# Kernel optimization log

Hardware: AMD Instinct MI355X
Metric: run time of the kernel (lower is better)

Reference implementation:

```python
import jax, jax.numpy as jnp
from jax import lax
import numpy as np


def gru_last(seq, Wih, Whh, bih, bhh):
    """Run a torch-style GRU over seq [N, T, C] and return only h_T [N, H].

    Gate order matches torch.nn.GRU: (r, z, n);
    n = tanh(W_in x + b_in + r * (W_hn h + b_hn)).
    """
    N = seq.shape[0]
    H = Whh.shape[1]

    def step(h, x_t):
        gi = x_t @ Wih.T + bih          # [N, 3H]
        gh = h @ Whh.T + bhh            # [N, 3H]
        i_r, i_z, i_n = jnp.split(gi, 3, axis=-1)
        h_r, h_z, h_n = jnp.split(gh, 3, axis=-1)
        r = jax.nn.sigmoid(i_r + h_r)
        z = jax.nn.sigmoid(i_z + h_z)
        n = jnp.tanh(i_n + r * h_n)
        h_new = (1.0 - z) * n + z * h
        return h_new, None

    h0 = jnp.zeros((N, H), dtype=seq.dtype)
    hT, _ = lax.scan(step, h0, jnp.swapaxes(seq, 0, 1))  # scan over T
    return hT


def setup_inputs() -> dict:
    key = jax.random.key(0)
    ks = jax.random.split(key, 12)
    B, C, T, Fq, H = 8, 64, 256, 256, 128
    s = 0.05
    return {
        "x": jax.random.normal(ks[0], (B, C, T, Fq), dtype=jnp.float32),
        "Wih_t": jax.random.normal(ks[1], (3 * H, C), dtype=jnp.float32) * s,
        "Whh_t": jax.random.normal(ks[2], (3 * H, H), dtype=jnp.float32) * s,
        "bih_t": jax.random.normal(ks[3], (3 * H,), dtype=jnp.float32) * s,
        "bhh_t": jax.random.normal(ks[4], (3 * H,), dtype=jnp.float32) * s,
        "Wih_f": jax.random.normal(ks[5], (3 * H, C), dtype=jnp.float32) * s,
        "Whh_f": jax.random.normal(ks[6], (3 * H, H), dtype=jnp.float32) * s,
        "bih_f": jax.random.normal(ks[7], (3 * H,), dtype=jnp.float32) * s,
        "bhh_f": jax.random.normal(ks[8], (3 * H,), dtype=jnp.float32) * s,
        "Wp": jax.random.normal(ks[9], (C, H), dtype=jnp.float32) * s,
        "bp": jax.random.normal(ks[10], (C,), dtype=jnp.float32) * s,
    }


def reference(x, Wih_t, Whh_t, bih_t, bhh_t, Wih_f, Whh_f, bih_f, bhh_f, Wp, bp):
    B, C, T, Fq = x.shape
    H = Whh_t.shape[1]

    # time GRU: sequences of length T, one per (batch, freq)
    t_in = jnp.transpose(x, (0, 3, 2, 1)).reshape(B * Fq, T, C)
    h_t = gru_last(t_in, Wih_t, Whh_t, bih_t, bhh_t)          # [B*F, H]
    t_vec = jnp.transpose(h_t.reshape(B, Fq, H), (0, 2, 1))    # [B, H, F]

    # freq GRU: sequences of length F, one per (batch, time)
    f_in = jnp.transpose(x, (0, 2, 3, 1)).reshape(B * T, Fq, C)
    h_f = gru_last(f_in, Wih_f, Whh_f, bih_f, bhh_f)          # [B*T, H]
    f_vec = jnp.transpose(h_f.reshape(B, T, H), (0, 2, 1))    # [B, H, T]

    # t_feat [B,H,F,1] expanded along dim2 to T (requires F == T),
    # f_feat [B,H,T,1] expanded along dim3 to F; fused is constant along F.
    s = t_vec + f_vec                                          # [B, H, T]  (F == T)
    out_t = jnp.einsum("ch,bht->bct", Wp, s) + bp[None, :, None]  # 1x1 conv
    return jnp.broadcast_to(out_t[:, :, :, None], (B, C, T, Fq))
```

## Files before the change

kernel.cpp:

```cpp
#include <hip/hip_runtime.h>

#define B_ 8
#define C_ 64
#define T_ 256
#define F_ 256
#define H_ 128
#define TF_ (T_*F_)

typedef _Float16 half_t;
typedef _Float16 half8 __attribute__((ext_vector_type(8)));
typedef float float4v __attribute__((ext_vector_type(4)));

#if __has_builtin(__builtin_amdgcn_exp2f)
#define EXP2F(x) __builtin_amdgcn_exp2f(x)
#else
static __device__ inline float EXP2F(float x) { float r; asm("v_exp_f32 %0, %1" : "=v"(r) : "v"(x)); return r; }
#endif
#if __has_builtin(__builtin_amdgcn_rcpf)
#define RCPF(x) __builtin_amdgcn_rcpf(x)
#else
static __device__ inline float RCPF(float x) { float r; asm("v_rcp_f32 %0, %1" : "=v"(r) : "v"(x)); return r; }
#endif

#define LDS_BARRIER() asm volatile("s_waitcnt lgkmcnt(0)\n\ts_barrier" ::: "memory")

#define NEG_L2E  (-1.4426950408889634f)
#define NEG_2L2E (-2.8853900817779268f)

__global__ __launch_bounds__(256) void k_transpose(const float* __restrict__ x,
                                                   half_t* __restrict__ xt) {
    __shared__ float lds[64 * 68];
    int blk = blockIdx.x;
    int b   = blk >> 10;
    int tf0 = (blk & 1023) << 6;
    int tid = threadIdx.x;
    int s = tid & 15;
    int q = tid >> 4;
    const float* xp = x + (size_t)(b * C_) * TF_ + tf0 + s * 4;
#pragma unroll
    for (int i = 0; i < 4; ++i) {
        int c = q + i * 16;
        float4v v = *(const float4v*)(xp + (size_t)c * TF_);
#pragma unroll
        for (int j = 0; j < 4; ++j) lds[(s * 4 + j) * 68 + c] = v[j];
    }
    __syncthreads();
    int row = tid >> 2;
    int c0  = (tid & 3) << 4;
    half8 o0, o1;
#pragma unroll
    for (int kq = 0; kq < 4; ++kq) {
        float4v v = *(const float4v*)&lds[row * 68 + c0 + kq * 4];
#pragma unroll
        for (int j = 0; j < 4; ++j) {
            if (kq < 2) o0[kq * 4 + j] = (half_t)v[j];
            else        o1[(kq - 2) * 4 + j] = (half_t)v[j];
        }
    }
    half_t* op = xt + ((size_t)b * TF_ + tf0 + row) * C_ + c0;
    *(half8*)op       = o0;
    *(half8*)(op + 8) = o1;
}

__device__ inline half8 load_w8s(const float* __restrict__ p, float s) {
    half8 r;
#pragma unroll
    for (int k = 0; k < 8; ++k) r[k] = (half_t)(p[k] * s);
    return r;
}

#define MFMA(a, b, c) __builtin_amdgcn_mfma_f32_16x16x32_f16((a), (b), (c), 0, 0, 0)

__global__ __launch_bounds__(512, 2) void k_gru(
    const half_t* __restrict__ xt,
    const float* __restrict__ Wih_t, const float* __restrict__ Whh_t,
    const float* __restrict__ bih_t, const float* __restrict__ bhh_t,
    const float* __restrict__ Wih_f, const float* __restrict__ Whh_f,
    const float* __restrict__ bih_f, const float* __restrict__ bhh_f,
    float* __restrict__ h_t_out, float* __restrict__ h_f_out) {
    __shared__ half_t hbuf0[16 * 136];
    __shared__ half_t hbuf1[16 * 136];

    int tid  = threadIdx.x;
    int w    = tid >> 6;
    int lane = tid & 63;
    int nidx = lane & 15;
    int quad = lane >> 4;

    int bi  = blockIdx.x;
    bool isf = bi >= 128;
    int lbi = bi & 127;
    int b   = lbi >> 4;
    int g16 = (lbi & 15) << 4;

    const float* Wih = isf ? Wih_f : Wih_t;
    const float* Whh = isf ? Whh_f : Whh_t;
    const float* bih = isf ? bih_f : bih_t;
    const float* bhh = isf ? bhh_f : bhh_t;
    float* hout      = isf ? h_f_out : h_t_out;

    size_t Sm = isf ? (size_t)(F_ * C_) : (size_t)C_;
    size_t Ss = isf ? (size_t)C_ : (size_t)(F_ * C_);
    size_t abase = (size_t)b * TF_ * C_ + (size_t)g16 * Sm;

    int gr = w * 16 + nidx;
    int gz = gr + 128;
    int gn = gr + 256;
    int ko = quad * 8;

    half8 wir0 = load_w8s(Wih + gr * 64 + ko,      NEG_L2E);
    half8 wir1 = load_w8s(Wih + gr * 64 + 32 + ko, NEG_L2E);
    half8 wiz0 = load_w8s(Wih + gz * 64 + ko,      NEG_L2E);
    half8 wiz1 = load_w8s(Wih + gz * 64 + 32 + ko, NEG_L2E);
    half8 win0 = load_w8s(Wih + gn * 64 + ko,      NEG_2L2E);
    half8 win1 = load_w8s(Wih + gn * 64 + 32 + ko, NEG_2L2E);
    half8 whr[4], whz[4], whn[4];
#pragma unroll
    for (int kt = 0; kt < 4; ++kt) {
        whr[kt] = load_w8s(Whh + gr * 128 + kt * 32 + ko, NEG_L2E);
        whz[kt] = load_w8s(Whh + gz * 128 + kt * 32 + ko, NEG_L2E);
        whn[kt] = load_w8s(Whh + gn * 128 + kt * 32 + ko, NEG_2L2E);
    }
    float br  = NEG_L2E  * (bih[gr] + bhh[gr]);
    float bz  = NEG_L2E  * (bih[gz] + bhh[gz]);
    float bin = NEG_2L2E * bih[gn];
    float bhn = NEG_2L2E * bhh[gn];

    for (int idx = tid; idx < 16 * 136; idx += 512) hbuf0[idx] = (half_t)0.f;
    float h_old[4] = {0.f, 0.f, 0.f, 0.f};

    const half_t* ap = xt + abase + (size_t)nidx * Sm + ko;
    half8 xA0 = *(const half8*)ap;
    half8 xA1 = *(const half8*)(ap + 32);
    ap += Ss;
    half8 xB0 = *(const half8*)ap;
    half8 xB1 = *(const half8*)(ap + 32);
    ap += Ss;

    float4v xr = {br, br, br, br};
    float4v xz = {bz, bz, bz, bz};
    float4v xn = {bin, bin, bin, bin};
    xr = MFMA(xA0, wir0, xr); xr = MFMA(xA1, wir1, xr);
    xz = MFMA(xA0, wiz0, xz); xz = MFMA(xA1, wiz1, xz);
    xn = MFMA(xA0, win0, xn); xn = MFMA(xA1, win1, xn);
    LDS_BARRIER();

#define GRU_STEP(RBUF, WBUF, XC0, XC1, XP0, XP1)                                \
    {                                                                           \
        const half_t* hrow = (RBUF) + nidx * 136 + ko;                          \
        half8 ha0 = *(const half8*)(hrow);                                      \
        half8 ha1 = *(const half8*)(hrow + 32);                                 \
        half8 ha2 = *(const half8*)(hrow + 64);                                 \
        half8 ha3 = *(const half8*)(hrow + 96);                                 \
        XP0 = *(const half8*)ap;                                                \
        XP1 = *(const half8*)(ap + 32);                                         \
        ap += Ss;                                                               \
        float4v hr  = {0.f, 0.f, 0.f, 0.f};                                     \
        float4v hz  = {0.f, 0.f, 0.f, 0.f};                                     \
        float4v hna = {bhn, bhn, bhn, bhn};                                     \
        float4v hnb = {0.f, 0.f, 0.f, 0.f};                                     \
        xr  = MFMA(ha0, whr[0], xr);  xr  = MFMA(ha1, whr[1], xr);              \
        hr  = MFMA(ha2, whr[2], hr);  hr  = MFMA(ha3, whr[3], hr);              \
        xz  = MFMA(ha0, whz[0], xz);  xz  = MFMA(ha1, whz[1], xz);              \
        hz  = MFMA(ha2, whz[2], hz);  hz  = MFMA(ha3, whz[3], hz);              \
        hna = MFMA(ha0, whn[0], hna); hna = MFMA(ha1, whn[1], hna);             \
        hnb = MFMA(ha2, whn[2], hnb); hnb = MFMA(ha3, whn[3], hnb);             \
        _Pragma("unroll")                                                       \
        for (int rg = 0; rg < 4; ++rg) {                                        \
            float r  = RCPF(1.f + EXP2F(xr[rg] + hr[rg]));                      \
            float z  = RCPF(1.f + EXP2F(xz[rg] + hz[rg]));                      \
            float np = xn[rg] + r * (hna[rg] + hnb[rg]);                        \
            float n  = 2.f * RCPF(1.f + EXP2F(np)) - 1.f;                       \
            float h  = n + z * (h_old[rg] - n);                                 \
            h_old[rg] = h;                                                      \
            (WBUF)[(quad * 4 + rg) * 136 + w * 16 + nidx] = (half_t)h;          \
        }                                                                       \
              \
        xr[0] = br;  xr[1] = br;  xr[2] = br;  xr[3] = br;                      \
        xz[0] = bz;  xz[1] = bz;  xz[2] = bz;  xz[3] = bz;                      \
        xn[0] = bin; xn[1] = bin; xn[2] = bin; xn[3] = bin;                     \
        xr = MFMA(XC0, wir0, xr); xr = MFMA(XC1, wir1, xr);                     \
        xz = MFMA(XC0, wiz0, xz); xz = MFMA(XC1, wiz1, xz);                     \
        xn = MFMA(XC0, win0, xn); xn = MFMA(XC1, win1, xn);                     \
        LDS_BARRIER();                                                          \
    }

    for (int it = 0; it < 128; ++it) {
        GRU_STEP(hbuf0, hbuf1, xB0, xB1, xA0, xA1)
        GRU_STEP(hbuf1, hbuf0, xA0, xA1, xB0, xB1)
    }
#undef GRU_STEP

    int srow = (b << 8) + g16;
#pragma unroll
    for (int rg = 0; rg < 4; ++rg) {
        hout[(size_t)(srow + quad * 4 + rg) * H_ + w * 16 + nidx] = h_old[rg];
    }
}

__global__ __launch_bounds__(256) void k_out(const float* __restrict__ h_t,
                                             const float* __restrict__ h_f,
                                             const float* __restrict__ Wp,
                                             const float* __restrict__ bp,
                                             float* __restrict__ out) {
    __shared__ float sv[128];
    __shared__ float part[4][64];
    __shared__ float orow[64];
    int blk = blockIdx.x;
    int b = blk >> 8;
    int i = blk & 255;
    int tid = threadIdx.x;
    size_t hoff = ((size_t)(b * 256 + i)) * 128;
    if (tid < 128) sv[tid] = h_t[hoff + tid] + h_f[hoff + tid];
    __syncthreads();
    int c = tid & 63;
    int q = tid >> 6;
    float p = 0.f;
    const float* wp = Wp + c * 128 + q * 32;
#pragma unroll
    for (int k = 0; k < 32; ++k) p += wp[k] * sv[q * 32 + k];
    part[q][c] = p;
    __syncthreads();
    if (tid < 64) orow[tid] = part[0][tid] + part[1][tid] + part[2][tid] + part[3][tid] + bp[tid];
    __syncthreads();
    int wv   = tid >> 6;
    int lane = tid & 63;
#pragma unroll
    for (int itr = 0; itr < 16; ++itr) {
        int cc = itr * 4 + wv;
        float v = orow[cc];
        float4v vv = {v, v, v, v};
        *(float4v*)(out + (((size_t)(b * 64 + cc)) * 256 + i) * 256 + lane * 4) = vv;
    }
}

extern "C" void kernel_launch(void* const* d_in, const int* in_sizes, int n_in,
                              void* d_out, int out_size, void* d_ws, size_t ws_size,
                              hipStream_t stream) {
    const float* x     = (const float*)d_in[0];
    const float* Wih_t = (const float*)d_in[1];
    const float* Whh_t = (const float*)d_in[2];
    const float* bih_t = (const float*)d_in[3];
    const float* bhh_t = (const float*)d_in[4];
    const float* Wih_f = (const float*)d_in[5];
    const float* Whh_f = (const float*)d_in[6];
    const float* bih_f = (const float*)d_in[7];
    const float* bhh_f = (const float*)d_in[8];
    const float* Wp    = (const float*)d_in[9];
    const float* bp    = (const float*)d_in[10];
    float* out = (float*)d_out;

    half_t* xt     = (half_t*)d_out;
    float* h_t_out = (float*)((char*)d_ws);
    float* h_f_out = (float*)((char*)d_ws + (size_t)2048 * 128 * 4);

    k_transpose<<<8192, 256, 0, stream>>>(x, xt);
    k_gru<<<256, 512, 0, stream>>>(xt, Wih_t, Whh_t, bih_t, bhh_t,
                                   Wih_f, Whh_f, bih_f, bhh_f, h_t_out, h_f_out);
    k_out<<<2048, 256, 0, stream>>>(h_t_out, h_f_out, Wp, bp, out);
}
```

Before: 437.8 us.

## Transpose MFMA operands and double-buffer input projections to overlap with gate math

Swaps the MFMA A/B operands so each lane holds four consecutive hidden units of one sequence. This allows per-lane vector bias loads, a single 4-wide half store of h into LDS, and a vectorized final store. The next step's input-projection MFMAs now issue before the gate nonlinearities, using ping-pong accumulators, so they can overlap with the transcendental math instead of sitting after it on the critical path. This costs extra registers for the second set of accumulators, which could hurt occupancy at 2 blocks of 512 threads.

New measurement: 439.5 us. About the same (+0.4%).

```diff
diff --git a/kernel.cpp b/kernel.cpp
--- a/kernel.cpp
+++ b/kernel.cpp
@@ -9,6 +9,7 @@
 
 typedef _Float16 half_t;
 typedef _Float16 half8 __attribute__((ext_vector_type(8)));
+typedef _Float16 half4v __attribute__((ext_vector_type(4)));
 typedef float float4v __attribute__((ext_vector_type(4)));
 
 #if __has_builtin(__builtin_amdgcn_exp2f)
@@ -86,6 +87,7 @@
     int lane = tid & 63;
     int nidx = lane & 15;
     int quad = lane >> 4;
+    int ko   = quad * 8;
 
     int bi  = blockIdx.x;
     bool isf = bi >= 128;
@@ -106,7 +108,6 @@
     int gr = w * 16 + nidx;
     int gz = gr + 128;
     int gn = gr + 256;
-    int ko = quad * 8;
 
     half8 wir0 = load_w8s(Wih + gr * 64 + ko,      NEG_L2E);
     half8 wir1 = load_w8s(Wih + gr * 64 + 32 + ko, NEG_L2E);
@@ -121,10 +122,12 @@
         whz[kt] = load_w8s(Whh + gz * 128 + kt * 32 + ko, NEG_L2E);
         whn[kt] = load_w8s(Whh + gn * 128 + kt * 32 + ko, NEG_2L2E);
     }
-    float br  = NEG_L2E  * (bih[gr] + bhh[gr]);
-    float bz  = NEG_L2E  * (bih[gz] + bhh[gz]);
-    float bin = NEG_2L2E * bih[gn];
-    float bhn = NEG_2L2E * bhh[gn];
+
+    int grb = w * 16 + quad * 4;
+    float4v brv  = (*(const float4v*)(bih + grb)       + *(const float4v*)(bhh + grb))       * NEG_L2E;
+    float4v bzv  = (*(const float4v*)(bih + grb + 128) + *(const float4v*)(bhh + grb + 128)) * NEG_L2E;
+    float4v binv = (*(const float4v*)(bih + grb + 256)) * NEG_2L2E;
+    float4v bhnv = (*(const float4v*)(bhh + grb + 256)) * NEG_2L2E;
 
     for (int idx = tid; idx < 16 * 136; idx += 512) hbuf0[idx] = (half_t)0.f;
     float h_old[4] = {0.f, 0.f, 0.f, 0.f};
@@ -137,15 +140,15 @@
     half8 xB1 = *(const half8*)(ap + 32);
     ap += Ss;
 
-    float4v xr = {br, br, br, br};
-    float4v xz = {bz, bz, bz, bz};
-    float4v xn = {bin, bin, bin, bin};
-    xr = MFMA(xA0, wir0, xr); xr = MFMA(xA1, wir1, xr);
-    xz = MFMA(xA0, wiz0, xz); xz = MFMA(xA1, wiz1, xz);
-    xn = MFMA(xA0, win0, xn); xn = MFMA(xA1, win1, xn);
+    float4v xrA = MFMA(wir0, xA0, brv);  xrA = MFMA(wir1, xA1, xrA);
+    float4v xzA = MFMA(wiz0, xA0, bzv);  xzA = MFMA(wiz1, xA1, xzA);
+    float4v xnA = MFMA(win0, xA0, binv); xnA = MFMA(win1, xA1, xnA);
+    float4v xrB, xzB, xnB;
     LDS_BARRIER();
 
-#define GRU_STEP(RBUF, WBUF, XC0, XC1, XP0, XP1)                                \
+    const float4v zero4 = {0.f, 0.f, 0.f, 0.f};
+
+#define GRU_STEP(RBUF, WBUF, XRC, XZC, XNC, XRF, XZF, XNF, XC0, XC1, XP0, XP1)  \
     {                                                                           \
         const half_t* hrow = (RBUF) + nidx * 136 + ko;                          \
         half8 ha0 = *(const half8*)(hrow);                                      \
@@ -155,47 +158,40 @@
         XP0 = *(const half8*)ap;                                                \
         XP1 = *(const half8*)(ap + 32);                                         \
         ap += Ss;                                                               \
-        float4v hr  = {0.f, 0.f, 0.f, 0.f};                                     \
-        float4v hz  = {0.f, 0.f, 0.f, 0.f};                                     \
-        float4v hna = {bhn, bhn, bhn, bhn};                                     \
-        float4v hnb = {0.f, 0.f, 0.f, 0.f};                                     \
-        xr  = MFMA(ha0, whr[0], xr);  xr  = MFMA(ha1, whr[1], xr);              \
-        hr  = MFMA(ha2, whr[2], hr);  hr  = MFMA(ha3, whr[3], hr);              \
-        xz  = MFMA(ha0, whz[0], xz);  xz  = MFMA(ha1, whz[1], xz);              \
-        hz  = MFMA(ha2, whz[2], hz);  hz  = MFMA(ha3, whz[3], hz);              \
-        hna = MFMA(ha0, whn[0], hna); hna = MFMA(ha1, whn[1], hna);             \
-        hnb = MFMA(ha2, whn[2], hnb); hnb = MFMA(ha3, whn[3], hnb);             \
+        float4v grv = MFMA(whr[0], ha0, XRC);  grv = MFMA(whr[1], ha1, grv);    \
+        float4v rp  = MFMA(whr[2], ha2, zero4); rp = MFMA(whr[3], ha3, rp);     \
+        float4v gzv = MFMA(whz[0], ha0, XZC);  gzv = MFMA(whz[1], ha1, gzv);    \
+        float4v zp  = MFMA(whz[2], ha2, zero4); zp = MFMA(whz[3], ha3, zp);     \
+        float4v na  = MFMA(whn[0], ha0, bhnv); na  = MFMA(whn[1], ha1, na);     \
+        float4v nb  = MFMA(whn[2], ha2, zero4); nb = MFMA(whn[3], ha3, nb);     \
+        \
+        XRF = MFMA(wir0, XC0, brv);  XRF = MFMA(wir1, XC1, XRF);                \
+        XZF = MFMA(wiz0, XC0, bzv);  XZF = MFMA(wiz1, XC1, XZF);                \
+        XNF = MFMA(win0, XC0, binv); XNF = MFMA(win1, XC1, XNF);                \
+        half4v hw;                                                              \
         _Pragma("unroll")                                                       \
         for (int rg = 0; rg < 4; ++rg) {                                        \
-            float r  = RCPF(1.f + EXP2F(xr[rg] + hr[rg]));                      \
-            float z  = RCPF(1.f + EXP2F(xz[rg] + hz[rg]));                      \
-            float np = xn[rg] + r * (hna[rg] + hnb[rg]);                        \
+            float r  = RCPF(1.f + EXP2F(grv[rg] + rp[rg]));                     \
+            float np = XNC[rg] + r * (na[rg] + nb[rg]);                         \
             float n  = 2.f * RCPF(1.f + EXP2F(np)) - 1.f;                       \
+            float z  = RCPF(1.f + EXP2F(gzv[rg] + zp[rg]));                     \
             float h  = n + z * (h_old[rg] - n);                                 \
             h_old[rg] = h;                                                      \
-            (WBUF)[(quad * 4 + rg) * 136 + w * 16 + nidx] = (half_t)h;          \
+            hw[rg] = (half_t)h;                                                 \
         }                                                                       \
-              \
-        xr[0] = br;  xr[1] = br;  xr[2] = br;  xr[3] = br;                      \
-        xz[0] = bz;  xz[1] = bz;  xz[2] = bz;  xz[3] = bz;                      \
-        xn[0] = bin; xn[1] = bin; xn[2] = bin; xn[3] = bin;                     \
-        xr = MFMA(XC0, wir0, xr); xr = MFMA(XC1, wir1, xr);                     \
-        xz = MFMA(XC0, wiz0, xz); xz = MFMA(XC1, wiz1, xz);                     \
-        xn = MFMA(XC0, win0, xn); xn = MFMA(XC1, win1, xn);                     \
+        *(half4v*)((WBUF) + nidx * 136 + w * 16 + quad * 4) = hw;               \
         LDS_BARRIER();                                                          \
     }
 
     for (int it = 0; it < 128; ++it) {
-        GRU_STEP(hbuf0, hbuf1, xB0, xB1, xA0, xA1)
-        GRU_STEP(hbuf1, hbuf0, xA0, xA1, xB0, xB1)
+        GRU_STEP(hbuf0, hbuf1, xrA, xzA, xnA, xrB, xzB, xnB, xB0, xB1, xA0, xA1)
+        GRU_STEP(hbuf1, hbuf0, xrB, xzB, xnB, xrA, xzA, xnA, xA0, xA1, xB0, xB1)
     }
 #undef GRU_STEP
 
     int srow = (b << 8) + g16;
-#pragma unroll
-    for (int rg = 0; rg < 4; ++rg) {
-        hout[(size_t)(srow + quad * 4 + rg) * H_ + w * 16 + nidx] = h_old[rg];
-    }
+    float4v hv = {h_old[0], h_old[1], h_old[2], h_old[3]};
+    *(float4v*)(hout + (size_t)(srow + nidx) * H_ + w * 16 + quad * 4) = hv;
 }
 
 __global__ __launch_bounds__(256) void k_out(const float* __restrict__ h_t,
```
